# Optimization experiments

Hardware: AMD Instinct MI355X
Metric: run time of the kernel (lower is better)

The kernel has to match this reference:

```python
import jax, jax.numpy as jnp
import numpy as np

B, N, D, H, T = 2048, 128, 256, 8, 64
HD = D // H
TANH_C = 10.0
MASK_PENALTY = 1e9


def setup_inputs() -> dict:
    key = jax.random.key(0)
    ks = jax.random.split(key, 16)
    s = 1.0 / np.sqrt(D).astype(np.float32)
    w = lambda k: jax.random.normal(k, (D, D), jnp.float32) * s
    return {
        'node_emb': jax.random.normal(ks[0], (B, N, D), jnp.float32),
        'graph_emb': jax.random.normal(ks[1], (B, D), jnp.float32),
        'W_target': w(ks[2]), 'W_global': w(ks[3]),
        'W_K1': w(ks[4]), 'W_K2': w(ks[5]),
        'W_Q': w(ks[6]), 'W_V': w(ks[7]),
        'Wq_m': w(ks[8]), 'Wk_m': w(ks[9]), 'Wv_m': w(ks[10]), 'Wo_m': w(ks[11]),
        'targets': jax.random.randint(ks[12], (T, B), 0, N, jnp.int32),
        'masks': jax.random.randint(ks[13], (T, B, N), 0, 2, jnp.int32),
    }


def _mha(q, k, v, Wq, Wk, Wv, Wo):
    # q: [B,1,D]; k,v: [B,N,D]. Standard multi-head attention (glimpse).
    qh = (q @ Wq.T).reshape(B, 1, H, HD).transpose(0, 2, 1, 3)   # [B,H,1,HD]
    kh = (k @ Wk.T).reshape(B, N, H, HD).transpose(0, 2, 1, 3)   # [B,H,N,HD]
    vh = (v @ Wv.T).reshape(B, N, H, HD).transpose(0, 2, 1, 3)
    scores = jnp.einsum('bhqd,bhnd->bhqn', qh, kh) / np.sqrt(HD).astype(np.float32)
    attn = jax.nn.softmax(scores, axis=-1)
    out = jnp.einsum('bhqn,bhnd->bhqd', attn, vh)                # [B,H,1,HD]
    out = out.transpose(0, 2, 1, 3).reshape(B, 1, D)
    return out @ Wo.T


def reference(node_emb, graph_emb, W_target, W_global, W_K1, W_K2, W_Q, W_V,
              Wq_m, Wk_m, Wv_m, Wo_m, targets, masks):
    # Step-invariant projections (embeddings fixed across decode steps here).
    keys = node_emb @ W_K1.T      # [B,N,D]
    vals = node_emb @ W_V.T       # [B,N,D]
    key2 = node_emb @ W_K2.T      # [B,N,D]
    g_ctx = graph_emb @ W_global.T  # [B,D]
    inv_sqrt_d = np.float32(1.0 / np.sqrt(D))

    def step(ll, tm):
        tgt, mask = tm  # tgt:[B] int32, mask:[B,N] int32
        tgt_emb = jnp.take_along_axis(node_emb, tgt[:, None, None], axis=1)[:, 0, :]  # [B,D]
        context = (tgt_emb @ W_target.T + g_ctx)[:, None, :]      # [B,1,D]
        glimpse = _mha(context, keys, vals, Wq_m, Wk_m, Wv_m, Wo_m)  # [B,1,D]
        query = glimpse @ W_Q.T                                    # [B,1,D]
        logits = jnp.einsum('bqd,bnd->bn', query, key2) * inv_sqrt_d  # [B,N]
        logits = TANH_C * jnp.tanh(logits) - mask.astype(jnp.float32) * MASK_PENALTY
        log_p = jax.nn.log_softmax(logits, axis=1)
        actions = jnp.argmax(log_p, axis=1)                        # greedy TopKSampler
        ll = ll + jnp.take_along_axis(log_p, actions[:, None], axis=1)[:, 0]
        return ll, None

    ll, _ = jax.lax.scan(step, jnp.zeros(B, jnp.float32), (targets, masks))
    return ll
```

## Files before the change

kernel.cpp:

```cpp
#include <hip/hip_runtime.h>
#include <hip/hip_bf16.h>

#define BB 2048
#define NN 128
#define DD 256
#define HH 8
#define TT 64

typedef __bf16 bf16x8 __attribute__((ext_vector_type(8)));
typedef float f32x4 __attribute__((ext_vector_type(4)));

static __device__ __forceinline__ f32x4 mfma16(bf16x8 a, bf16x8 b, f32x4 c) {
  return __builtin_amdgcn_mfma_f32_16x16x32_bf16(a, b, c, 0, 0, 0);
}

static __device__ __forceinline__ f32x4 zero4() {
  f32x4 z = {0.f, 0.f, 0.f, 0.f};
  return z;
}

static __device__ __forceinline__ bf16x8 cvt8(const float* p) {
  const float4 x0 = *(const float4*)p;
  const float4 x1 = *(const float4*)(p + 4);
  bf16x8 r;
  r[0] = (__bf16)x0.x; r[1] = (__bf16)x0.y; r[2] = (__bf16)x0.z; r[3] = (__bf16)x0.w;
  r[4] = (__bf16)x1.x; r[5] = (__bf16)x1.y; r[6] = (__bf16)x1.z; r[7] = (__bf16)x1.w;
  return r;
}

static __device__ __forceinline__ unsigned pk2(float a, float b) {
  __bf16 x = (__bf16)a, y = (__bf16)b;
  unsigned short ux, uy;
  __builtin_memcpy(&ux, &x, 2);
  __builtin_memcpy(&uy, &y, 2);
  return (unsigned)ux | ((unsigned)uy << 16);
}

static __device__ __forceinline__ float fast_tanh10(float y) {
  const float e = __expf(2.f * y);
  return 10.f - 20.f * __builtin_amdgcn_rcpf(1.f + e);
}

__global__ void fold1(const float* __restrict__ Wq_m, const float* __restrict__ W_target,
                      const float* __restrict__ W_global, const float* __restrict__ Wk_m,
                      const float* __restrict__ W_K1, const float* __restrict__ Wv_m,
                      const float* __restrict__ W_V, const float* __restrict__ W_Q,
                      const float* __restrict__ Wo_m,
                      __bf16* __restrict__ WTQ, float* __restrict__ WGQT,
                      __bf16* __restrict__ WKH, __bf16* __restrict__ WVH,
                      float* __restrict__ WQO) {
  const int p = blockIdx.x >> 8;
  const int i = blockIdx.x & 255;
  const int t = threadIdx.x;
  __shared__ float arow[256];
  const float* A;
  const float* Bm;
  if (p == 0)      { A = Wq_m; Bm = W_target; }
  else if (p == 1) { A = Wq_m; Bm = W_global; }
  else if (p == 2) { A = Wk_m; Bm = W_K1; }
  else if (p == 3) { A = Wv_m; Bm = W_V; }
  else             { A = W_Q;  Bm = Wo_m; }
  arow[t] = A[i * 256 + t];
  __syncthreads();
  float acc = 0.f;
  for (int k = 0; k < 256; ++k) acc = fmaf(arow[k], Bm[k * 256 + t], acc);
  if (p == 0)      WTQ[i * 256 + t] = (__bf16)acc;
  else if (p == 1) WGQT[t * 256 + i] = acc;
  else if (p == 2) WKH[i * 256 + t] = (__bf16)acc;
  else if (p == 3) WVH[i * 256 + t] = (__bf16)acc;
  else             WQO[i * 256 + t] = acc;
}

__global__ void fold2(const float* __restrict__ WQO, const float* __restrict__ W_K2,
                      __bf16* __restrict__ WZL) {
  const int j = blockIdx.x;
  const int t = threadIdx.x;
  __shared__ float col[256];
  col[t] = W_K2[t * 256 + j];
  __syncthreads();
  float acc = 0.f;
  for (int d = 0; d < 256; ++d) acc = fmaf(WQO[d * 256 + t], col[d], acc);
  WZL[j * 256 + t] = (__bf16)acc;
}

__global__ void gq_kernel(const float* __restrict__ ge, const float* __restrict__ WGQT,
                          float* __restrict__ GQ) {
  const int b0 = blockIdx.x * 8;
  const int t = threadIdx.x;
  __shared__ float g[8][256];
#pragma unroll
  for (int i = 0; i < 8; ++i) g[i][t] = ge[(b0 + i) * 256 + t];
  __syncthreads();
  float acc[8] = {0.f, 0.f, 0.f, 0.f, 0.f, 0.f, 0.f, 0.f};
  for (int j = 0; j < 256; ++j) {
    const float wv = WGQT[j * 256 + t];
#pragma unroll
    for (int i = 0; i < 8; ++i) acc[i] = fmaf(wv, g[i][j], acc[i]);
  }
#pragma unroll
  for (int i = 0; i < 8; ++i) GQ[(b0 + i) * 256 + t] = acc[i];
}

__global__ __launch_bounds__(512)
void kvq_kernel(const float* __restrict__ E, const int* __restrict__ tg,
                const __bf16* __restrict__ WKH, const __bf16* __restrict__ WVH,
                const __bf16* __restrict__ WTQ, const float* __restrict__ GQ,
                __bf16* __restrict__ KH, __bf16* __restrict__ VT,
                __bf16* __restrict__ Qb, __bf16* __restrict__ Ebf) {
  const int b = blockIdx.x;
  const int tid = threadIdx.x;
  const int w = tid >> 6;
  const int l = tid & 63;
  const int lr = l & 15;
  const int lg = l >> 4;
  __shared__ __align__(16) __bf16 Es[128 * 264];
  __shared__ int tgs[64];
  if (tid < 64) tgs[tid] = tg[tid * BB + b];
  const float* Eb = E + (size_t)b * NN * DD;
  __bf16* Ebfb = Ebf + (size_t)b * NN * DD;
#pragma unroll
  for (int it = 0; it < 8; ++it) {
    const int c = it * 512 + tid;
    const int row = c >> 5;
    const int c8 = c & 31;
    const bf16x8 v = cvt8(Eb + row * 256 + c8 * 8);
    *(bf16x8*)&Es[row * 264 + c8 * 8] = v;
    *(bf16x8*)(Ebfb + row * 256 + c8 * 8) = v;
  }
  __syncthreads();

  {
    f32x4 acc[8][2];
#pragma unroll
    for (int mf = 0; mf < 8; ++mf)
#pragma unroll
      for (int nf = 0; nf < 2; ++nf) acc[mf][nf] = zero4();
    for (int kk = 0; kk < 8; ++kk) {
      bf16x8 aF[8], bF[2];
#pragma unroll
      for (int mf = 0; mf < 8; ++mf)
        aF[mf] = *(const bf16x8*)&Es[(mf * 16 + lr) * 264 + kk * 32 + lg * 8];
#pragma unroll
      for (int nf = 0; nf < 2; ++nf)
        bF[nf] = *(const bf16x8*)(WKH + (size_t)(w * 32 + nf * 16 + lr) * DD + kk * 32 + lg * 8);
#pragma unroll
      for (int mf = 0; mf < 8; ++mf)
#pragma unroll
        for (int nf = 0; nf < 2; ++nf) acc[mf][nf] = mfma16(aF[mf], bF[nf], acc[mf][nf]);
    }
    __bf16* KHb = KH + (size_t)b * NN * DD;
#pragma unroll
    for (int mf = 0; mf < 8; ++mf)
#pragma unroll
      for (int nf = 0; nf < 2; ++nf)
#pragma unroll
        for (int r = 0; r < 4; ++r)
          KHb[(mf * 16 + lg * 4 + r) * DD + w * 32 + nf * 16 + lr] = (__bf16)acc[mf][nf][r];
  }

  {
    f32x4 acc[2][8];
#pragma unroll
    for (int mf = 0; mf < 2; ++mf)
#pragma unroll
      for (int nf = 0; nf < 8; ++nf) acc[mf][nf] = zero4();
    for (int kk = 0; kk < 8; ++kk) {
      bf16x8 aW[2], bE[8];
#pragma unroll
      for (int mf = 0; mf < 2; ++mf)
        aW[mf] = *(const bf16x8*)(WVH + (size_t)(w * 32 + mf * 16 + lr) * DD + kk * 32 + lg * 8);
#pragma unroll
      for (int nf = 0; nf < 8; ++nf)
        bE[nf] = *(const bf16x8*)&Es[(nf * 16 + lr) * 264 + kk * 32 + lg * 8];
#pragma unroll
      for (int mf = 0; mf < 2; ++mf)
#pragma unroll
        for (int nf = 0; nf < 8; ++nf) acc[mf][nf] = mfma16(aW[mf], bE[nf], acc[mf][nf]);
    }
    __bf16* VTb = VT + (size_t)b * DD * NN;
#pragma unroll
    for (int mf = 0; mf < 2; ++mf)
#pragma unroll
      for (int nf = 0; nf < 8; ++nf)
#pragma unroll
        for (int r = 0; r < 4; ++r)
          VTb[(w * 32 + mf * 16 + lg * 4 + r) * NN + nf * 16 + lr] = (__bf16)acc[mf][nf][r];
  }

  {
    f32x4 acc[4][2];
#pragma unroll
    for (int mf = 0; mf < 4; ++mf)
#pragma unroll
      for (int nf = 0; nf < 2; ++nf) acc[mf][nf] = zero4();
    int rowoff[4];
#pragma unroll
    for (int mf = 0; mf < 4; ++mf) rowoff[mf] = tgs[mf * 16 + lr] * 264;
    for (int kk = 0; kk < 8; ++kk) {
      bf16x8 aF[4], bF[2];
#pragma unroll
      for (int mf = 0; mf < 4; ++mf)
        aF[mf] = *(const bf16x8*)&Es[rowoff[mf] + kk * 32 + lg * 8];
#pragma unroll
      for (int nf = 0; nf < 2; ++nf)
        bF[nf] = *(const bf16x8*)(WTQ + (size_t)(w * 32 + nf * 16 + lr) * DD + kk * 32 + lg * 8);
#pragma unroll
      for (int mf = 0; mf < 4; ++mf)
#pragma unroll
        for (int nf = 0; nf < 2; ++nf) acc[mf][nf] = mfma16(aF[mf], bF[nf], acc[mf][nf]);
    }
#pragma unroll
    for (int nf = 0; nf < 2; ++nf) {
      const int col = w * 32 + nf * 16 + lr;
      const float g = GQ[b * DD + col];
#pragma unroll
      for (int mf = 0; mf < 4; ++mf)
#pragma unroll
        for (int r = 0; r < 4; ++r)
          Qb[((size_t)b * TT + mf * 16 + lg * 4 + r) * DD + col] = (__bf16)(acc[mf][nf][r] + g);
    }
  }
}

__global__ __launch_bounds__(256)
void attn4_kernel(const __bf16* __restrict__ Qb, const __bf16* __restrict__ KH,
                  const __bf16* __restrict__ VT, __bf16* __restrict__ HO) {
  const int b = blockIdx.x >> 2;
  const int c0 = (blockIdx.x & 3) * 64;
  const int tid = threadIdx.x;
  const int w = tid >> 6;
  const int l = tid & 63;
  const int lr = l & 15;
  const int lg = l >> 4;
  const int T0 = w * 16;

  __shared__ __align__(16) __bf16 KHs[128 * 72];
  __shared__ __align__(16) __bf16 VTs[64 * 136];
  __shared__ __align__(16) __bf16 Ps[4][16 * 136];

  const __bf16* KHb = KH + (size_t)b * NN * DD;
  const __bf16* VTb = VT + (size_t)b * DD * NN;

#pragma unroll
  for (int it = 0; it < 4; ++it) {
    const int c = it * 256 + tid;
    const int row = c >> 3;
    const int c8 = c & 7;
    *(bf16x8*)&KHs[row * 72 + c8 * 8] = *(const bf16x8*)(KHb + (size_t)row * DD + c0 + c8 * 8);
  }
#pragma unroll
  for (int it = 0; it < 4; ++it) {
    const int c = it * 256 + tid;
    const int row = c >> 4;
    const int c8 = c & 15;
    *(bf16x8*)&VTs[row * 136 + c8 * 8] =
        *(const bf16x8*)(VTb + (size_t)(c0 + row) * NN + c8 * 8);
  }
  __syncthreads();

  __bf16* myp = Ps[w];
  __bf16* HOb = HO + (size_t)b * TT * DD + c0;

#pragma unroll
  for (int h = 0; h < 2; ++h) {
    const bf16x8 aq =
        *(const bf16x8*)(Qb + ((size_t)b * TT + T0 + lr) * DD + c0 + h * 32 + lg * 8);
    f32x4 s[8];
#pragma unroll
    for (int nf = 0; nf < 8; ++nf)
      s[nf] = mfma16(*(const bf16x8*)&KHs[(nf * 16 + lr) * 72 + h * 32 + lg * 8], aq, zero4());

    float mx = -1e30f;
#pragma unroll
    for (int nf = 0; nf < 8; ++nf)
#pragma unroll
      for (int r = 0; r < 4; ++r) mx = fmaxf(mx, s[nf][r]);
    mx = fmaxf(mx, __shfl_xor(mx, 16));
    mx = fmaxf(mx, __shfl_xor(mx, 32));

    float sm = 0.f;
    uint2 evp[8];
#pragma unroll
    for (int nf = 0; nf < 8; ++nf) {
      const float e0 = __expf((s[nf][0] - mx) * 0.17677669529663687f);
      const float e1 = __expf((s[nf][1] - mx) * 0.17677669529663687f);
      const float e2 = __expf((s[nf][2] - mx) * 0.17677669529663687f);
      const float e3 = __expf((s[nf][3] - mx) * 0.17677669529663687f);
      sm += (e0 + e1) + (e2 + e3);
      evp[nf].x = pk2(e0, e1);
      evp[nf].y = pk2(e2, e3);
    }
    sm += __shfl_xor(sm, 16);
    sm += __shfl_xor(sm, 32);

#pragma unroll
    for (int nf = 0; nf < 8; ++nf)
      *(uint2*)&myp[lr * 136 + nf * 16 + lg * 4] = evp[nf];

    f32x4 o0 = zero4(), o1 = zero4();
#pragma unroll
    for (int kk = 0; kk < 4; ++kk) {
      const bf16x8 ap = *(const bf16x8*)&myp[lr * 136 + kk * 32 + lg * 8];
      o0 = mfma16(ap, *(const bf16x8*)&VTs[(h * 32 + lr) * 136 + kk * 32 + lg * 8], o0);
      o1 = mfma16(ap, *(const bf16x8*)&VTs[(h * 32 + 16 + lr) * 136 + kk * 32 + lg * 8], o1);
    }
#pragma unroll
    for (int r = 0; r < 4; ++r) {
      const float inv = __builtin_amdgcn_rcpf(__shfl(sm, lg * 4 + r));
      HOb[(size_t)(T0 + lg * 4 + r) * DD + h * 32 + lr] = (__bf16)(o0[r] * inv);
      HOb[(size_t)(T0 + lg * 4 + r) * DD + h * 32 + 16 + lr] = (__bf16)(o1[r] * inv);
    }
  }
}

__global__ __launch_bounds__(256)
void zlog2_kernel(const __bf16* __restrict__ Ebf, const __bf16* __restrict__ HO,
                  const __bf16* __restrict__ WZL, const int* __restrict__ MK,
                  float* __restrict__ out) {
  const int b = blockIdx.x;
  const int tid = threadIdx.x;
  const int w = tid >> 6;
  const int l = tid & 63;
  const int lr = l & 15;
  const int lg = l >> 4;
  const int T0 = w * 16;
  __shared__ __align__(16) __bf16 Zs[64 * 264];
  __shared__ float red[4];

  const __bf16* Eb = Ebf + (size_t)b * NN * DD;
  const __bf16* HOb = HO + (size_t)b * TT * DD;

  {
    f32x4 acc[4][4];
#pragma unroll
    for (int mf = 0; mf < 4; ++mf)
#pragma unroll
      for (int nf = 0; nf < 4; ++nf) acc[mf][nf] = zero4();
    for (int kk = 0; kk < 8; ++kk) {
      bf16x8 aF[4], bF[4];
#pragma unroll
      for (int mf = 0; mf < 4; ++mf)
        aF[mf] = *(const bf16x8*)(HOb + (size_t)(mf * 16 + lr) * DD + kk * 32 + lg * 8);
#pragma unroll
      for (int nf = 0; nf < 4; ++nf)
        bF[nf] = *(const bf16x8*)(WZL + (size_t)(w * 64 + nf * 16 + lr) * DD + kk * 32 + lg * 8);
#pragma unroll
      for (int mf = 0; mf < 4; ++mf)
#pragma unroll
        for (int nf = 0; nf < 4; ++nf) acc[mf][nf] = mfma16(aF[mf], bF[nf], acc[mf][nf]);
    }
#pragma unroll
    for (int mf = 0; mf < 4; ++mf)
#pragma unroll
      for (int nf = 0; nf < 4; ++nf)
#pragma unroll
        for (int r = 0; r < 4; ++r)
          Zs[(mf * 16 + lg * 4 + r) * 264 + w * 64 + nf * 16 + lr] = (__bf16)acc[mf][nf][r];
  }
  __syncthreads();

  {
    f32x4 sa[8];
#pragma unroll
    for (int nf = 0; nf < 8; ++nf) sa[nf] = zero4();
    for (int kk = 0; kk < 8; ++kk) {
      const bf16x8 bZ = *(const bf16x8*)&Zs[(T0 + lr) * 264 + kk * 32 + lg * 8];
#pragma unroll
      for (int nf = 0; nf < 8; ++nf) {
        const bf16x8 aE = *(const bf16x8*)(Eb + (size_t)(nf * 16 + lr) * DD + kk * 32 + lg * 8);
        sa[nf] = mfma16(aE, bZ, sa[nf]);
      }
    }
    const int t = T0 + lr;
    float xs[8][4];
    float mx = -3e38f;
#pragma unroll
    for (int nf = 0; nf < 8; ++nf) {
      const int4 mk4 = *(const int4*)(MK + ((size_t)t * BB + b) * NN + nf * 16 + lg * 4);
      xs[nf][0] = fast_tanh10(sa[nf][0] * 0.0625f) - (float)mk4.x * 1e9f;
      xs[nf][1] = fast_tanh10(sa[nf][1] * 0.0625f) - (float)mk4.y * 1e9f;
      xs[nf][2] = fast_tanh10(sa[nf][2] * 0.0625f) - (float)mk4.z * 1e9f;
      xs[nf][3] = fast_tanh10(sa[nf][3] * 0.0625f) - (float)mk4.w * 1e9f;
      mx = fmaxf(mx, fmaxf(fmaxf(xs[nf][0], xs[nf][1]), fmaxf(xs[nf][2], xs[nf][3])));
    }
    mx = fmaxf(mx, __shfl_xor(mx, 16));
    mx = fmaxf(mx, __shfl_xor(mx, 32));
    float sm = 0.f;
#pragma unroll
    for (int nf = 0; nf < 8; ++nf)
#pragma unroll
      for (int r = 0; r < 4; ++r) sm += __expf(xs[nf][r] - mx);
    sm += __shfl_xor(sm, 16);
    sm += __shfl_xor(sm, 32);
    float part = logf(sm);
    part += __shfl_xor(part, 1);
    part += __shfl_xor(part, 2);
    part += __shfl_xor(part, 4);
    part += __shfl_xor(part, 8);
    if (l == 0) red[w] = part;
  }
  __syncthreads();
  if (tid == 0) out[b] = -(red[0] + red[1] + red[2] + red[3]);
}

extern "C" void kernel_launch(void* const* d_in, const int* in_sizes, int n_in,
                              void* d_out, int out_size, void* d_ws, size_t ws_size,
                              hipStream_t stream) {
  (void)in_sizes; (void)n_in; (void)out_size; (void)ws_size;
  const float* node_emb  = (const float*)d_in[0];
  const float* graph_emb = (const float*)d_in[1];
  const float* W_target  = (const float*)d_in[2];
  const float* W_global  = (const float*)d_in[3];
  const float* W_K1      = (const float*)d_in[4];
  const float* W_K2      = (const float*)d_in[5];
  const float* W_Q       = (const float*)d_in[6];
  const float* W_V       = (const float*)d_in[7];
  const float* Wq_m      = (const float*)d_in[8];
  const float* Wk_m      = (const float*)d_in[9];
  const float* Wv_m      = (const float*)d_in[10];
  const float* Wo_m      = (const float*)d_in[11];
  const int* targets     = (const int*)d_in[12];
  const int* masks       = (const int*)d_in[13];

  char* p = (char*)d_ws;
  __bf16* Ebf = (__bf16*)p; p += (size_t)BB * NN * DD * 2;
  __bf16* KH  = (__bf16*)p; p += (size_t)BB * NN * DD * 2;
  __bf16* VT  = (__bf16*)p; p += (size_t)BB * DD * NN * 2;
  __bf16* HO  = (__bf16*)p; p += (size_t)BB * TT * DD * 2;
  __bf16* Qb  = (__bf16*)p; p += (size_t)BB * TT * DD * 2;
  __bf16* WTQ = (__bf16*)p; p += 256 * 256 * 2;
  __bf16* WKH = (__bf16*)p; p += 256 * 256 * 2;
  __bf16* WVH = (__bf16*)p; p += 256 * 256 * 2;
  __bf16* WZL = (__bf16*)p; p += 256 * 256 * 2;
  float* WGQT = (float*)p;  p += 256 * 256 * 4;
  float* WQO  = (float*)p;  p += 256 * 256 * 4;
  float* GQ   = (float*)p;  p += (size_t)BB * DD * 4;

  fold1<<<1280, 256, 0, stream>>>(Wq_m, W_target, W_global, Wk_m, W_K1, Wv_m, W_V, W_Q, Wo_m,
                                  WTQ, WGQT, WKH, WVH, WQO);
  fold2<<<256, 256, 0, stream>>>(WQO, W_K2, WZL);
  gq_kernel<<<BB / 8, 256, 0, stream>>>(graph_emb, WGQT, GQ);
  kvq_kernel<<<BB, 512, 0, stream>>>(node_emb, targets, WKH, WVH, WTQ, GQ, KH, VT, Qb, Ebf);
  attn4_kernel<<<BB * 4, 256, 0, stream>>>(Qb, KH, VT, HO);
  zlog2_kernel<<<BB, 256, 0, stream>>>(Ebf, HO, WZL, masks, (float*)d_out);
}
```

Before: 513.2 us.

## Pre-transpose masks to byte layout and unroll MFMA k-loops

After: 572.6 us. +11.6%, slower.

```diff
diff --git a/kernel.cpp b/kernel.cpp
--- a/kernel.cpp
+++ b/kernel.cpp
@@ -101,7 +101,21 @@
   for (int i = 0; i < 8; ++i) GQ[(b0 + i) * 256 + t] = acc[i];
 }
 
-__global__ __launch_bounds__(512)
+__global__ void mkt_kernel(const int* __restrict__ MK, unsigned char* __restrict__ MKT) {
+  const int t = blockIdx.x >> 3;
+  const int b = ((blockIdx.x & 7) << 8) + threadIdx.x;
+  const int* src = MK + ((size_t)t * BB + b) * NN;
+  unsigned char* dst = MKT + ((size_t)b << 13) + (t << 7);
+#pragma unroll
+  for (int c = 0; c < 32; ++c) {
+    const int4 v = *(const int4*)(src + c * 4);
+    const unsigned pk = (unsigned)(v.x & 1) | ((unsigned)(v.y & 1) << 8) |
+                        ((unsigned)(v.z & 1) << 16) | ((unsigned)(v.w & 1) << 24);
+    *(unsigned*)(dst + c * 4) = pk;
+  }
+}
+
+__global__ __launch_bounds__(512, 4)
 void kvq_kernel(const float* __restrict__ E, const int* __restrict__ tg,
                 const __bf16* __restrict__ WKH, const __bf16* __restrict__ WVH,
                 const __bf16* __restrict__ WTQ, const float* __restrict__ GQ,
@@ -135,6 +149,7 @@
     for (int mf = 0; mf < 8; ++mf)
 #pragma unroll
       for (int nf = 0; nf < 2; ++nf) acc[mf][nf] = zero4();
+#pragma unroll
     for (int kk = 0; kk < 8; ++kk) {
       bf16x8 aF[8], bF[2];
 #pragma unroll
@@ -164,6 +179,7 @@
     for (int mf = 0; mf < 2; ++mf)
 #pragma unroll
       for (int nf = 0; nf < 8; ++nf) acc[mf][nf] = zero4();
+#pragma unroll
     for (int kk = 0; kk < 8; ++kk) {
       bf16x8 aW[2], bE[8];
 #pragma unroll
@@ -196,6 +212,7 @@
     int rowoff[4];
 #pragma unroll
     for (int mf = 0; mf < 4; ++mf) rowoff[mf] = tgs[mf * 16 + lr] * 264;
+#pragma unroll
     for (int kk = 0; kk < 8; ++kk) {
       bf16x8 aF[4], bF[2];
 #pragma unroll
@@ -315,7 +332,7 @@
 
 __global__ __launch_bounds__(256)
 void zlog2_kernel(const __bf16* __restrict__ Ebf, const __bf16* __restrict__ HO,
-                  const __bf16* __restrict__ WZL, const int* __restrict__ MK,
+                  const __bf16* __restrict__ WZL, const unsigned char* __restrict__ MKT,
                   float* __restrict__ out) {
   const int b = blockIdx.x;
   const int tid = threadIdx.x;
@@ -336,6 +353,7 @@
     for (int mf = 0; mf < 4; ++mf)
 #pragma unroll
       for (int nf = 0; nf < 4; ++nf) acc[mf][nf] = zero4();
+#pragma unroll
     for (int kk = 0; kk < 8; ++kk) {
       bf16x8 aF[4], bF[4];
 #pragma unroll
@@ -363,6 +381,7 @@
     f32x4 sa[8];
 #pragma unroll
     for (int nf = 0; nf < 8; ++nf) sa[nf] = zero4();
+#pragma unroll
     for (int kk = 0; kk < 8; ++kk) {
       const bf16x8 bZ = *(const bf16x8*)&Zs[(T0 + lr) * 264 + kk * 32 + lg * 8];
 #pragma unroll
@@ -372,15 +391,16 @@
       }
     }
     const int t = T0 + lr;
+    const unsigned char* mrow = MKT + ((size_t)b << 13) + ((size_t)t << 7);
     float xs[8][4];
     float mx = -3e38f;
 #pragma unroll
     for (int nf = 0; nf < 8; ++nf) {
-      const int4 mk4 = *(const int4*)(MK + ((size_t)t * BB + b) * NN + nf * 16 + lg * 4);
-      xs[nf][0] = fast_tanh10(sa[nf][0] * 0.0625f) - (float)mk4.x * 1e9f;
-      xs[nf][1] = fast_tanh10(sa[nf][1] * 0.0625f) - (float)mk4.y * 1e9f;
-      xs[nf][2] = fast_tanh10(sa[nf][2] * 0.0625f) - (float)mk4.z * 1e9f;
-      xs[nf][3] = fast_tanh10(sa[nf][3] * 0.0625f) - (float)mk4.w * 1e9f;
+      const unsigned mkw = *(const unsigned*)(mrow + nf * 16 + lg * 4);
+      xs[nf][0] = fast_tanh10(sa[nf][0] * 0.0625f) - (float)(mkw & 0xff) * 1e9f;
+      xs[nf][1] = fast_tanh10(sa[nf][1] * 0.0625f) - (float)((mkw >> 8) & 0xff) * 1e9f;
+      xs[nf][2] = fast_tanh10(sa[nf][2] * 0.0625f) - (float)((mkw >> 16) & 0xff) * 1e9f;
+      xs[nf][3] = fast_tanh10(sa[nf][3] * 0.0625f) - (float)((mkw >> 24) & 0xff) * 1e9f;
       mx = fmaxf(mx, fmaxf(fmaxf(xs[nf][0], xs[nf][1]), fmaxf(xs[nf][2], xs[nf][3])));
     }
     mx = fmaxf(mx, __shfl_xor(mx, 16));
@@ -428,6 +448,7 @@
   __bf16* VT  = (__bf16*)p; p += (size_t)BB * DD * NN * 2;
   __bf16* HO  = (__bf16*)p; p += (size_t)BB * TT * DD * 2;
   __bf16* Qb  = (__bf16*)p; p += (size_t)BB * TT * DD * 2;
+  unsigned char* MKT = (unsigned char*)p; p += (size_t)BB * TT * NN;
   __bf16* WTQ = (__bf16*)p; p += 256 * 256 * 2;
   __bf16* WKH = (__bf16*)p; p += 256 * 256 * 2;
   __bf16* WVH = (__bf16*)p; p += 256 * 256 * 2;
@@ -440,7 +461,8 @@
                                   WTQ, WGQT, WKH, WVH, WQO);
   fold2<<<256, 256, 0, stream>>>(WQO, W_K2, WZL);
   gq_kernel<<<BB / 8, 256, 0, stream>>>(graph_emb, WGQT, GQ);
+  mkt_kernel<<<TT * 8, 256, 0, stream>>>(masks, MKT);
   kvq_kernel<<<BB, 512, 0, stream>>>(node_emb, targets, WKH, WVH, WTQ, GQ, KH, VT, Qb, Ebf);
   attn4_kernel<<<BB * 4, 256, 0, stream>>>(Qb, KH, VT, HO);
-  zlog2_kernel<<<BB, 256, 0, stream>>>(Ebf, HO, WZL, masks, (float*)d_out);
-}
+  zlog2_kernel<<<BB, 256, 0, stream>>>(Ebf, HO, WZL, MKT, (float*)d_out);
+}
```
